# Optimization experiments

Hardware: AMD Instinct MI355X
Metric: run time of the kernel (lower is better)

Reference implementation:

```python
import jax, jax.numpy as jnp
import numpy as np


def setup_inputs() -> dict:
    key = jax.random.key(0)
    k1, k2 = jax.random.split(key)
    B, DIM, T, SIZE = 64, 512, 2048, 1024
    H = jax.random.normal(k1, (B, DIM, T), dtype=jnp.float32)
    units = jax.random.normal(k2, (DIM, SIZE), dtype=jnp.float32)
    return {"H": H, "units": units}


def reference(H, units):
    # H: (B, dim, T), units: (dim, size)
    # Original: C[b, s, t] = exp(-||H[b,:,t] - units[:,s]||^2) normalized over s.
    # exp(-d^2) / sum_s exp(-d^2) == softmax(-d^2, axis=s).
    Ht = jnp.swapaxes(H, 1, 2)                      # (B, T, dim)
    h_sq = jnp.sum(Ht * Ht, axis=-1, keepdims=True)  # (B, T, 1)
    m_sq = jnp.sum(units * units, axis=0)            # (size,)
    cross = jnp.einsum('btd,ds->bts', Ht, units)     # (B, T, size) GEMM
    sqdist = h_sq - 2.0 * cross + m_sq               # (B, T, size)
    C = jax.nn.softmax(-sqdist, axis=-1)             # normalize over codebook
    return jnp.swapaxes(C, 1, 2)                     # (B, size, T)
```

## Files before the change

### kernel.cpp

```cpp
#include <hip/hip_runtime.h>
#include <stdint.h>


typedef unsigned short u16;
typedef __attribute__((ext_vector_type(8))) short short8;
typedef __attribute__((ext_vector_type(4))) float f32x4;
typedef __attribute__((ext_vector_type(16))) float f32x16;

#define B_DIM 64
#define DIM   512
#define T_DIM 2048
#define S_DIM 1024

#define B_LO_O 65536
#define REDM_O 131072
#define REDS_O 133120
#define SM_SZ  135168

__device__ __forceinline__ u16 f32_to_bf16(float f) {
  uint32_t u = __float_as_uint(f);
  uint32_t r = u + 0x7FFFu + ((u >> 16) & 1u);
  return (u16)(r >> 16);
}
__device__ __forceinline__ float bf16_to_f32(u16 h) {
  return __uint_as_float(((uint32_t)h) << 16);
}

__global__ __launch_bounds__(256) void k_prep_units(const float* __restrict__ units,
                                                    u16* __restrict__ UpH, u16* __restrict__ UpL,
                                                    float* __restrict__ msq) {
  const int s0 = blockIdx.x * 4;
  const int tid = threadIdx.x;
  const int lane = tid & 63, wv = tid >> 6;
  float acc0 = 0.f, acc1 = 0.f, acc2 = 0.f, acc3 = 0.f;
#pragma unroll
  for (int j = 0; j < 2; ++j) {
    const int d = tid + j * 256;
    const float4 v = *(const float4*)(units + (size_t)d * S_DIM + s0);
    acc0 += v.x * v.x; acc1 += v.y * v.y; acc2 += v.z * v.z; acc3 += v.w * v.w;
    const int dbase = (d >> 4) * 16384 + ((d >> 3) & 1) * 256 + (d & 7);
    const float fv[4] = {v.x, v.y, v.z, v.w};
#pragma unroll
    for (int q = 0; q < 4; ++q) {
      const int s = s0 + q;
      const int idx = dbase + ((s >> 5) * 64 + (s & 31)) * 8;
      const u16 h = f32_to_bf16(fv[q]);
      UpH[idx] = h;
      UpL[idx] = f32_to_bf16(fv[q] - bf16_to_f32(h));
    }
  }
#pragma unroll
  for (int off = 1; off < 64; off <<= 1) {
    acc0 += __shfl_xor(acc0, off);
    acc1 += __shfl_xor(acc1, off);
    acc2 += __shfl_xor(acc2, off);
    acc3 += __shfl_xor(acc3, off);
  }
  __shared__ float part[4][4];
  if (lane == 0) { part[wv][0] = acc0; part[wv][1] = acc1; part[wv][2] = acc2; part[wv][3] = acc3; }
  __syncthreads();
  if (tid < 4) msq[s0 + tid] = part[0][tid] + part[1][tid] + part[2][tid] + part[3][tid];
}

__global__ __launch_bounds__(256) void k_prep_h(const float* __restrict__ H,
                                                u16* __restrict__ BpH, u16* __restrict__ BpL) {
  __shared__ float tile[64 * 68];
  const int bx = blockIdx.x;
  const int d0 = blockIdx.y * 64;
  const int b = blockIdx.z;
  const int t0 = bx * 64;
  const int tid = threadIdx.x;
#pragma unroll
  for (int j = 0; j < 4; ++j) {
    const int chunk = tid + j * 256;
    const int r = chunk >> 4, c4 = (chunk & 15) * 4;
    const float4 v = *(const float4*)(H + ((size_t)(b * DIM + d0 + r)) * T_DIM + t0 + c4);
    *(float4*)(&tile[r * 68 + c4]) = v;
  }
  __syncthreads();
#pragma unroll
  for (int j = 0; j < 2; ++j) {
    const int chunk = tid + j * 256;
    const int q = chunk >> 3, e8 = (chunk & 7) * 8;
    union { u16 us[8]; uint4 v4; } hi, lo;
#pragma unroll
    for (int k = 0; k < 8; ++k) {
      const float f = tile[(e8 + k) * 68 + q];
      const u16 h = f32_to_bf16(f);
      hi.us[k] = h;
      lo.us[k] = f32_to_bf16(f - bf16_to_f32(h));
    }
    const int dg = d0 + e8;
    const int chunkB = (q >> 5) * 64 + ((dg >> 3) & 1) * 32 + (q & 31);
    const size_t o = ((((size_t)b * 32 + bx) * 32 + (dg >> 4)) * 128 + chunkB) * 8;
    *(uint4*)(BpH + o) = hi.v4;
    *(uint4*)(BpL + o) = lo.v4;
  }
}

__device__ __forceinline__ void gl16(const void* g, void* l) {
  __builtin_amdgcn_global_load_lds((const __attribute__((address_space(1))) void*)g,
                                   (__attribute__((address_space(3))) void*)l, 16, 0, 0);
}

#define WAITV0() asm volatile("s_waitcnt vmcnt(0)" ::: "memory")
#define SYNCPT() do { __builtin_amdgcn_s_barrier(); __builtin_amdgcn_sched_barrier(0); } while (0)

__global__ __launch_bounds__(512, 2) void k_fused(const u16* __restrict__ UpH, const u16* __restrict__ UpL,
                                                  const u16* __restrict__ BpH, const u16* __restrict__ BpL,
                                                  const float* __restrict__ msq,
                                                  float* __restrict__ out) {
  __shared__ __align__(16) char sm[SM_SZ];
  const int tid = threadIdx.x;
  const int lane = tid & 63, wv = tid >> 6;
  const int l31 = lane & 31, lhi = lane >> 5;
  const int sw = wv;

  const int tgx = blockIdx.x;
  const int t00 = tgx * 64;
  const int bb = blockIdx.y;

  const char* const aH = (const char*)UpH + (sw * 4) * 1024 + lane * 16;
  const char* const aL = (const char*)UpL + (sw * 4) * 1024 + lane * 16;
  const size_t bgBase = (((size_t)bb * 32 + tgx) * 32) * 2048;
  const char* const pBH = (const char*)BpH + bgBase;
  const char* const pBL = (const char*)BpL + bgBase;

  f32x16 acc[4][2];
#pragma unroll
  for (int mt = 0; mt < 4; ++mt)
#pragma unroll
    for (int nt = 0; nt < 2; ++nt)
#pragma unroll
      for (int r = 0; r < 16; ++r)
        acc[mt][nt][r] = 0.f;

  short8 ah0[4], ah1[4], al0[4], al1[4];
  short8 bh0[2], bh1[2], bl0[2], bl1[2];

#define LD_AH(D, KS) do { const size_t ko = (size_t)(KS) * 32768;            \
    (D)[0] = *(const short8*)(aH + ko);                                      \
    (D)[1] = *(const short8*)(aH + ko + 1024);                               \
    (D)[2] = *(const short8*)(aH + ko + 2048);                               \
    (D)[3] = *(const short8*)(aH + ko + 3072); } while (0)
#define LD_AL(D, KS) do { const size_t ko = (size_t)(KS) * 32768;            \
    (D)[0] = *(const short8*)(aL + ko);                                      \
    (D)[1] = *(const short8*)(aL + ko + 1024);                               \
    (D)[2] = *(const short8*)(aL + ko + 2048);                               \
    (D)[3] = *(const short8*)(aL + ko + 3072); } while (0)
#define DS_B(BH, BL, KS) do { const int bo = (KS) * 2048 + lane * 16;        \
    (BH)[0] = *(const short8*)(sm + bo);                                     \
    (BH)[1] = *(const short8*)(sm + bo + 1024);                              \
    (BL)[0] = *(const short8*)(sm + B_LO_O + bo);                            \
    (BL)[1] = *(const short8*)(sm + B_LO_O + bo + 1024); } while (0)
#define STG(J) do { const int off = (16 + 2 * (J)) * 2048 + (wv & 3) * 1024 + lane * 16; \
    if (wv < 4) gl16(pBH + off, sm + off);                                   \
    else        gl16(pBL + off, sm + B_LO_O + off); } while (0)

#define MM8(AF, BF)                                                          \
    __builtin_amdgcn_s_setprio(1);                                           \
    _Pragma("unroll") for (int mt = 0; mt < 4; ++mt)                         \
      _Pragma("unroll") for (int nt = 0; nt < 2; ++nt)                       \
        acc[mt][nt] = __builtin_amdgcn_mfma_f32_32x32x16_bf16((AF)[mt], (BF)[nt], acc[mt][nt], 0, 0, 0); \
    __builtin_amdgcn_s_setprio(0);

#pragma unroll
  for (int r = 0; r < 4; ++r) {
    const int off = (tid + r * 512) * 16;
    gl16(pBH + off, sm + off);
    gl16(pBL + off, sm + B_LO_O + off);
  }
  LD_AH(ah0, 0); LD_AL(al0, 0);
  WAITV0();
  SYNCPT();
  DS_B(bh0, bl0, 0);
  LD_AH(ah1, 1); LD_AL(al1, 1);
  DS_B(bh1, bl1, 1);

#pragma unroll 1
  for (int k = 0; k < 32; k += 2) {
    if (k == 10) { WAITV0(); SYNCPT(); }
    const int kc2 = (k + 2 < 32) ? (k + 2) : 31;
    const int kc3 = (k + 3 < 32) ? (k + 3) : 31;
    if (k < 8) STG(k);
    MM8(ah0, bh0);
    MM8(ah0, bl0);
    MM8(al0, bh0);
    LD_AH(ah0, kc2); LD_AL(al0, kc2); DS_B(bh0, bl0, kc2);
    if (k + 1 < 8) STG(k + 1);
    MM8(ah1, bh1);
    MM8(ah1, bl1);
    MM8(al1, bh1);
    LD_AH(ah1, kc3); LD_AL(al1, kc3); DS_B(bh1, bl1, kc3);
  }

  float* redM = (float*)(sm + REDM_O);
  float* redS = (float*)(sm + REDS_O);
  float mx0 = -3.0e38f, mx1 = -3.0e38f;
#pragma unroll
  for (int mt = 0; mt < 4; ++mt) {
    const int sb = sw * 128 + mt * 32 + lhi * 4;
#pragma unroll
    for (int q = 0; q < 4; ++q) {
      const f32x4 mq = *(const f32x4*)(msq + sb + q * 8);
#pragma unroll
      for (int r = 0; r < 4; ++r) {
        const int reg = q * 4 + r;
        const float v0 = 2.f * acc[mt][0][reg] - mq[r];
        const float v1 = 2.f * acc[mt][1][reg] - mq[r];
        acc[mt][0][reg] = v0; acc[mt][1][reg] = v1;
        mx0 = fmaxf(mx0, v0); mx1 = fmaxf(mx1, v1);
      }
    }
  }
  mx0 = fmaxf(mx0, __shfl_xor(mx0, 32));
  mx1 = fmaxf(mx1, __shfl_xor(mx1, 32));
  if (lane < 32) { redM[wv * 64 + l31] = mx0; redM[wv * 64 + 32 + l31] = mx1; }
  __syncthreads();
  float M0 = redM[l31], M1 = redM[32 + l31];
#pragma unroll
  for (int w = 1; w < 8; ++w) {
    M0 = fmaxf(M0, redM[w * 64 + l31]);
    M1 = fmaxf(M1, redM[w * 64 + 32 + l31]);
  }
  float s0 = 0.f, s1 = 0.f;
#pragma unroll
  for (int mt = 0; mt < 4; ++mt)
#pragma unroll
    for (int reg = 0; reg < 16; ++reg) {
      const float e0 = __expf(acc[mt][0][reg] - M0);
      const float e1 = __expf(acc[mt][1][reg] - M1);
      acc[mt][0][reg] = e0; acc[mt][1][reg] = e1;
      s0 += e0; s1 += e1;
    }
  s0 += __shfl_xor(s0, 32);
  s1 += __shfl_xor(s1, 32);
  if (lane < 32) { redS[wv * 64 + l31] = s0; redS[wv * 64 + 32 + l31] = s1; }
  __syncthreads();
  float S0 = redS[l31], S1 = redS[32 + l31];
#pragma unroll
  for (int w = 1; w < 8; ++w) {
    S0 += redS[w * 64 + l31];
    S1 += redS[w * 64 + 32 + l31];
  }
  const float r0 = 1.0f / S0, r1 = 1.0f / S1;

  float* const outb = out + ((size_t)bb << 21);
  const int tc0 = t00 + l31, tc1 = t00 + 32 + l31;
#pragma unroll
  for (int mt = 0; mt < 4; ++mt) {
    const int sb = sw * 128 + mt * 32 + lhi * 4;
#pragma unroll
    for (int q = 0; q < 4; ++q)
#pragma unroll
      for (int r = 0; r < 4; ++r) {
        const int srow = sb + q * 8 + r;
        const int reg = q * 4 + r;
        outb[(size_t)srow * T_DIM + tc0] = acc[mt][0][reg] * r0;
        outb[(size_t)srow * T_DIM + tc1] = acc[mt][1][reg] * r1;
      }
  }
}

extern "C" void kernel_launch(void* const* d_in, const int* in_sizes, int n_in,
                              void* d_out, int out_size, void* d_ws, size_t ws_size,
                              hipStream_t stream) {
  (void)in_sizes; (void)n_in; (void)out_size; (void)ws_size;
  const float* H = (const float*)d_in[0];
  const float* units = (const float*)d_in[1];
  float* out = (float*)d_out;
  char* ws = (char*)d_ws;
  u16* BpH = (u16*)(ws);
  u16* BpL = (u16*)(ws + 134217728);
  u16* UpH = (u16*)(ws + 268435456);
  u16* UpL = (u16*)(ws + 269484032);
  float* msq = (float*)(ws + 270532608);

  k_prep_units<<<dim3(S_DIM / 4), 256, 0, stream>>>(units, UpH, UpL, msq);
  k_prep_h<<<dim3(T_DIM / 64, DIM / 64, B_DIM), 256, 0, stream>>>(H, BpH, BpL);
  k_fused<<<dim3(T_DIM / 64, B_DIM), 512, 0, stream>>>(UpH, UpL, BpH, BpL, msq, out);
}
```

Before: 577.8 us.

## Restructure K-loop into per-slab pipeline with fine-grained vmcnt waits

Replaces the double-buffered B fragments and the single full vmcnt(0) drain at k==10 with a per-slab schedule. Each slab syncs, reads its B fragment from LDS, issues the next LDS stage, waits on lgkm, and interleaves the next A global loads between the MFMA groups. Counted vmcnt waits let each slab wait only for its own data instead of draining every outstanding load. In exchange it adds a barrier per slab and drops the B register prefetch, so LDS read latency is exposed before each slab's MFMAs. Correctness depends on the hand-counted vmcnt values being right.

```diff
diff --git a/kernel.cpp b/kernel.cpp
--- a/kernel.cpp
+++ b/kernel.cpp
@@ -103,8 +103,9 @@
                                    (__attribute__((address_space(3))) void*)l, 16, 0, 0);
 }
 
-#define WAITV0() asm volatile("s_waitcnt vmcnt(0)" ::: "memory")
+#define WAITV(N) asm volatile("s_waitcnt vmcnt(" #N ")" ::: "memory")
 #define SYNCPT() do { __builtin_amdgcn_s_barrier(); __builtin_amdgcn_sched_barrier(0); } while (0)
+#define LGKM0()  do { asm volatile("s_waitcnt lgkmcnt(0)" ::: "memory"); __builtin_amdgcn_sched_barrier(0); } while (0)
 
 __global__ __launch_bounds__(512, 2) void k_fused(const u16* __restrict__ UpH, const u16* __restrict__ UpL,
                                                   const u16* __restrict__ BpH, const u16* __restrict__ BpL,
@@ -136,7 +137,7 @@
         acc[mt][nt][r] = 0.f;
 
   short8 ah0[4], ah1[4], al0[4], al1[4];
-  short8 bh0[2], bh1[2], bl0[2], bl1[2];
+  short8 bh[2], bl[2];
 
 #define LD_AH(D, KS) do { const size_t ko = (size_t)(KS) * 32768;            \
     (D)[0] = *(const short8*)(aH + ko);                                      \
@@ -148,12 +149,12 @@
     (D)[1] = *(const short8*)(aL + ko + 1024);                               \
     (D)[2] = *(const short8*)(aL + ko + 2048);                               \
     (D)[3] = *(const short8*)(aL + ko + 3072); } while (0)
-#define DS_B(BH, BL, KS) do { const int bo = (KS) * 2048 + lane * 16;        \
-    (BH)[0] = *(const short8*)(sm + bo);                                     \
-    (BH)[1] = *(const short8*)(sm + bo + 1024);                              \
-    (BL)[0] = *(const short8*)(sm + B_LO_O + bo);                            \
-    (BL)[1] = *(const short8*)(sm + B_LO_O + bo + 1024); } while (0)
-#define STG(J) do { const int off = (16 + 2 * (J)) * 2048 + (wv & 3) * 1024 + lane * 16; \
+#define DS_B(KS) do { const int bo = (KS) * 2048 + lane * 16;                \
+    bh[0] = *(const short8*)(sm + bo);                                       \
+    bh[1] = *(const short8*)(sm + bo + 1024);                                \
+    bl[0] = *(const short8*)(sm + B_LO_O + bo);                              \
+    bl[1] = *(const short8*)(sm + B_LO_O + bo + 1024); } while (0)
+#define STG(K) do { const int off = (16 + 2 * (K)) * 2048 + (wv & 3) * 1024 + lane * 16; \
     if (wv < 4) gl16(pBH + off, sm + off);                                   \
     else        gl16(pBL + off, sm + B_LO_O + off); } while (0)
 
@@ -164,6 +165,18 @@
         acc[mt][nt] = __builtin_amdgcn_mfma_f32_32x32x16_bf16((AF)[mt], (BF)[nt], acc[mt][nt], 0, 0, 0); \
     __builtin_amdgcn_s_setprio(0);
 
+#define SLAB(K, AH, AL, DO_STG, DO_LD) do {                                  \
+    SYNCPT();                                                                \
+    DS_B(K);                                                                 \
+    if (DO_STG) STG(K);                                                      \
+    LGKM0();                                                                 \
+    MM8(AH, bh);                                                             \
+    MM8(AH, bl);                                                             \
+    if (DO_LD) LD_AH(AH, (K) + 2);                                           \
+    MM8(AL, bh);                                                             \
+    if (DO_LD) LD_AL(AL, (K) + 2);                                           \
+  } while (0)
+
 #pragma unroll
   for (int r = 0; r < 4; ++r) {
     const int off = (tid + r * 512) * 16;
@@ -171,28 +184,25 @@
     gl16(pBL + off, sm + B_LO_O + off);
   }
   LD_AH(ah0, 0); LD_AL(al0, 0);
-  WAITV0();
-  SYNCPT();
-  DS_B(bh0, bl0, 0);
   LD_AH(ah1, 1); LD_AL(al1, 1);
-  DS_B(bh1, bl1, 1);
-
+  WAITV(16);
+
+  WAITV(8);  SLAB(0, ah0, al0, true, true);
+  WAITV(9);  SLAB(1, ah1, al1, true, true);
 #pragma unroll 1
-  for (int k = 0; k < 32; k += 2) {
-    if (k == 10) { WAITV0(); SYNCPT(); }
-    const int kc2 = (k + 2 < 32) ? (k + 2) : 31;
-    const int kc3 = (k + 3 < 32) ? (k + 3) : 31;
-    if (k < 8) STG(k);
-    MM8(ah0, bh0);
-    MM8(ah0, bl0);
-    MM8(al0, bh0);
-    LD_AH(ah0, kc2); LD_AL(al0, kc2); DS_B(bh0, bl0, kc2);
-    if (k + 1 < 8) STG(k + 1);
-    MM8(ah1, bh1);
-    MM8(ah1, bl1);
-    MM8(al1, bh1);
-    LD_AH(ah1, kc3); LD_AL(al1, kc3); DS_B(bh1, bl1, kc3);
-  }
+  for (int k = 2; k < 8; k += 2) {
+    WAITV(9);  SLAB(k,     ah0, al0, true, true);
+    WAITV(9);  SLAB(k + 1, ah1, al1, true, true);
+  }
+  WAITV(9);  SLAB(8, ah0, al0, false, true);
+#pragma unroll 1
+  for (int k = 9; k < 29; k += 2) {
+    WAITV(8);  SLAB(k,     ah1, al1, false, true);
+    WAITV(8);  SLAB(k + 1, ah0, al0, false, true);
+  }
+  WAITV(8);  SLAB(29, ah1, al1, false, true);
+  WAITV(8);  SLAB(30, ah0, al0, false, false);
+  WAITV(0);  SLAB(31, ah1, al1, false, false);
 
   float* redM = (float*)(sm + REDM_O);
   float* redS = (float*)(sm + REDS_O);
```

Result: faster. 560.4 us (-3.0%).

## Restructure GEMM main loop into phased pipeline with fine-grained vmcnt waits

Applied to the files above, without the earlier changes.

Rewrites the K loop as 16 phases. Each phase synchronises, reads both B k-slices from LDS up front, and issues the global loads for the next A fragments between MFMA groups, gated by explicit partial vmcnt waits instead of a single full drain. The aim is to overlap global A-fragment latency and LDS staging with MFMA work, and to avoid the full vmcnt(0) stall at the staging boundary. In exchange there is a workgroup barrier every phase, and correctness now depends on hand-counted outstanding-load numbers.

```diff
diff --git a/kernel.cpp b/kernel.cpp
--- a/kernel.cpp
+++ b/kernel.cpp
@@ -103,8 +103,9 @@
                                    (__attribute__((address_space(3))) void*)l, 16, 0, 0);
 }
 
-#define WAITV0() asm volatile("s_waitcnt vmcnt(0)" ::: "memory")
+#define WAITV(N) asm volatile("s_waitcnt vmcnt(" #N ")" ::: "memory")
 #define SYNCPT() do { __builtin_amdgcn_s_barrier(); __builtin_amdgcn_sched_barrier(0); } while (0)
+#define LGKM0()  do { asm volatile("s_waitcnt lgkmcnt(0)" ::: "memory"); __builtin_amdgcn_sched_barrier(0); } while (0)
 
 __global__ __launch_bounds__(512, 2) void k_fused(const u16* __restrict__ UpH, const u16* __restrict__ UpL,
                                                   const u16* __restrict__ BpH, const u16* __restrict__ BpL,
@@ -135,8 +136,8 @@
       for (int r = 0; r < 16; ++r)
         acc[mt][nt][r] = 0.f;
 
-  short8 ah0[4], ah1[4], al0[4], al1[4];
-  short8 bh0[2], bh1[2], bl0[2], bl1[2];
+  short8 ahA[4], alA[4], ahB[4], alB[4];
+  short8 bhA[2], blA[2], bhB[2], blB[2];
 
 #define LD_AH(D, KS) do { const size_t ko = (size_t)(KS) * 32768;            \
     (D)[0] = *(const short8*)(aH + ko);                                      \
@@ -148,7 +149,7 @@
     (D)[1] = *(const short8*)(aL + ko + 1024);                               \
     (D)[2] = *(const short8*)(aL + ko + 2048);                               \
     (D)[3] = *(const short8*)(aL + ko + 3072); } while (0)
-#define DS_B(BH, BL, KS) do { const int bo = (KS) * 2048 + lane * 16;        \
+#define DS_B2(BH, BL, KS) do { const int bo = (KS) * 2048 + lane * 16;       \
     (BH)[0] = *(const short8*)(sm + bo);                                     \
     (BH)[1] = *(const short8*)(sm + bo + 1024);                              \
     (BL)[0] = *(const short8*)(sm + B_LO_O + bo);                            \
@@ -164,35 +165,46 @@
         acc[mt][nt] = __builtin_amdgcn_mfma_f32_32x32x16_bf16((AF)[mt], (BF)[nt], acc[mt][nt], 0, 0, 0); \
     __builtin_amdgcn_s_setprio(0);
 
+#define PHASE(J, DO_STG, WN) do {                                            \
+    const int s0_ = 2 * (J), s1_ = 2 * (J) + 1;                              \
+    const int p0_ = (s0_ + 2 < 32) ? s0_ + 2 : 31;                           \
+    const int p1_ = (s1_ + 2 < 32) ? s1_ + 2 : 31;                           \
+    SYNCPT();                                                                \
+    DS_B2(bhA, blA, s0_);                                                    \
+    DS_B2(bhB, blB, s1_);                                                    \
+    if (DO_STG) STG(J);                                                      \
+    LGKM0();                                                                 \
+    WAITV(WN);                                                               \
+    MM8(ahA, bhA);                                                           \
+    MM8(ahA, blA);                                                           \
+    LD_AH(ahA, p0_);                                                         \
+    WAITV(WN);                                                               \
+    MM8(alA, bhA);                                                           \
+    LD_AL(alA, p0_);                                                         \
+    WAITV(WN);                                                               \
+    MM8(ahB, bhB);                                                           \
+    MM8(ahB, blB);                                                           \
+    LD_AH(ahB, p1_);                                                         \
+    WAITV(WN);                                                               \
+    MM8(alB, bhB);                                                           \
+    LD_AL(alB, p1_);                                                         \
+  } while (0)
+
 #pragma unroll
   for (int r = 0; r < 4; ++r) {
     const int off = (tid + r * 512) * 16;
     gl16(pBH + off, sm + off);
     gl16(pBL + off, sm + B_LO_O + off);
   }
-  LD_AH(ah0, 0); LD_AL(al0, 0);
-  WAITV0();
-  SYNCPT();
-  DS_B(bh0, bl0, 0);
-  LD_AH(ah1, 1); LD_AL(al1, 1);
-  DS_B(bh1, bl1, 1);
-
+  LD_AH(ahA, 0); LD_AL(alA, 0);
+  LD_AH(ahB, 1); LD_AL(alB, 1);
+  WAITV(16);
+
+  PHASE(0, true, 13);
 #pragma unroll 1
-  for (int k = 0; k < 32; k += 2) {
-    if (k == 10) { WAITV0(); SYNCPT(); }
-    const int kc2 = (k + 2 < 32) ? (k + 2) : 31;
-    const int kc3 = (k + 3 < 32) ? (k + 3) : 31;
-    if (k < 8) STG(k);
-    MM8(ah0, bh0);
-    MM8(ah0, bl0);
-    MM8(al0, bh0);
-    LD_AH(ah0, kc2); LD_AL(al0, kc2); DS_B(bh0, bl0, kc2);
-    if (k + 1 < 8) STG(k + 1);
-    MM8(ah1, bh1);
-    MM8(ah1, bl1);
-    MM8(al1, bh1);
-    LD_AH(ah1, kc3); LD_AL(al1, kc3); DS_B(bh1, bl1, kc3);
-  }
+  for (int j = 1; j < 8; ++j) PHASE(j, true, 13);
+#pragma unroll 1
+  for (int j = 8; j < 16; ++j) PHASE(j, false, 12);
 
   float* redM = (float*)(sm + REDM_O);
   float* redS = (float*)(sm + REDS_O);
```

Measured after the change: 559.1 us. 1.03x faster.

## Split fused GEMM-softmax block across 16 waves with simpler unpipelined K loop

Applied to the files above, without the earlier changes.

The fused kernel now launches 1024 threads (16 waves) per block, and each wave owns 64 codebook rows instead of 128, which halves the per-wave accumulator and fragment register footprint. The staged, double-buffered K loop with interleaved partial B loads is replaced by one upfront load of the whole B tile into LDS, followed by a plain loop that reads A from global and B from LDS every step. The aim is to hide latency through more resident waves instead of software pipelining. In exchange, loads and MFMAs inside each wave are no longer overlapped, and the softmax reductions now span 16 waves.

```diff
diff --git a/kernel.cpp b/kernel.cpp
--- a/kernel.cpp
+++ b/kernel.cpp
@@ -14,8 +14,8 @@
 
 #define B_LO_O 65536
 #define REDM_O 131072
-#define REDS_O 133120
-#define SM_SZ  135168
+#define REDS_O 135168
+#define SM_SZ  139264
 
 __device__ __forceinline__ u16 f32_to_bf16(float f) {
   uint32_t u = __float_as_uint(f);
@@ -106,10 +106,10 @@
 #define WAITV0() asm volatile("s_waitcnt vmcnt(0)" ::: "memory")
 #define SYNCPT() do { __builtin_amdgcn_s_barrier(); __builtin_amdgcn_sched_barrier(0); } while (0)
 
-__global__ __launch_bounds__(512, 2) void k_fused(const u16* __restrict__ UpH, const u16* __restrict__ UpL,
-                                                  const u16* __restrict__ BpH, const u16* __restrict__ BpL,
-                                                  const float* __restrict__ msq,
-                                                  float* __restrict__ out) {
+__global__ __launch_bounds__(1024, 4) void k_fused(const u16* __restrict__ UpH, const u16* __restrict__ UpL,
+                                                   const u16* __restrict__ BpH, const u16* __restrict__ BpL,
+                                                   const float* __restrict__ msq,
+                                                   float* __restrict__ out) {
   __shared__ __align__(16) char sm[SM_SZ];
   const int tid = threadIdx.x;
   const int lane = tid & 63, wv = tid >> 6;
@@ -120,86 +120,69 @@
   const int t00 = tgx * 64;
   const int bb = blockIdx.y;
 
-  const char* const aH = (const char*)UpH + (sw * 4) * 1024 + lane * 16;
-  const char* const aL = (const char*)UpL + (sw * 4) * 1024 + lane * 16;
-  const size_t bgBase = (((size_t)bb * 32 + tgx) * 32) * 2048;
+  const char* const aH = (const char*)UpH + sw * 2048 + lane * 16;
+  const char* const aL = (const char*)UpL + sw * 2048 + lane * 16;
+  const size_t bgBase = (size_t)(bb * 32 + tgx) * 65536;
   const char* const pBH = (const char*)BpH + bgBase;
   const char* const pBL = (const char*)BpL + bgBase;
 
-  f32x16 acc[4][2];
-#pragma unroll
-  for (int mt = 0; mt < 4; ++mt)
+#pragma unroll
+  for (int r = 0; r < 4; ++r) {
+    const int off = (tid + r * 1024) * 16;
+    gl16(pBH + off, sm + off);
+  }
+#pragma unroll
+  for (int r = 0; r < 4; ++r) {
+    const int off = (tid + r * 1024) * 16;
+    gl16(pBL + off, sm + B_LO_O + off);
+  }
+
+  f32x16 acc[2][2];
+#pragma unroll
+  for (int mt = 0; mt < 2; ++mt)
 #pragma unroll
     for (int nt = 0; nt < 2; ++nt)
 #pragma unroll
       for (int r = 0; r < 16; ++r)
         acc[mt][nt][r] = 0.f;
 
-  short8 ah0[4], ah1[4], al0[4], al1[4];
-  short8 bh0[2], bh1[2], bl0[2], bl1[2];
-
-#define LD_AH(D, KS) do { const size_t ko = (size_t)(KS) * 32768;            \
-    (D)[0] = *(const short8*)(aH + ko);                                      \
-    (D)[1] = *(const short8*)(aH + ko + 1024);                               \
-    (D)[2] = *(const short8*)(aH + ko + 2048);                               \
-    (D)[3] = *(const short8*)(aH + ko + 3072); } while (0)
-#define LD_AL(D, KS) do { const size_t ko = (size_t)(KS) * 32768;            \
-    (D)[0] = *(const short8*)(aL + ko);                                      \
-    (D)[1] = *(const short8*)(aL + ko + 1024);                               \
-    (D)[2] = *(const short8*)(aL + ko + 2048);                               \
-    (D)[3] = *(const short8*)(aL + ko + 3072); } while (0)
-#define DS_B(BH, BL, KS) do { const int bo = (KS) * 2048 + lane * 16;        \
-    (BH)[0] = *(const short8*)(sm + bo);                                     \
-    (BH)[1] = *(const short8*)(sm + bo + 1024);                              \
-    (BL)[0] = *(const short8*)(sm + B_LO_O + bo);                            \
-    (BL)[1] = *(const short8*)(sm + B_LO_O + bo + 1024); } while (0)
-#define STG(J) do { const int off = (16 + 2 * (J)) * 2048 + (wv & 3) * 1024 + lane * 16; \
-    if (wv < 4) gl16(pBH + off, sm + off);                                   \
-    else        gl16(pBL + off, sm + B_LO_O + off); } while (0)
-
-#define MM8(AF, BF)                                                          \
-    __builtin_amdgcn_s_setprio(1);                                           \
-    _Pragma("unroll") for (int mt = 0; mt < 4; ++mt)                         \
-      _Pragma("unroll") for (int nt = 0; nt < 2; ++nt)                       \
-        acc[mt][nt] = __builtin_amdgcn_mfma_f32_32x32x16_bf16((AF)[mt], (BF)[nt], acc[mt][nt], 0, 0, 0); \
-    __builtin_amdgcn_s_setprio(0);
-
-#pragma unroll
-  for (int r = 0; r < 4; ++r) {
-    const int off = (tid + r * 512) * 16;
-    gl16(pBH + off, sm + off);
-    gl16(pBL + off, sm + B_LO_O + off);
-  }
-  LD_AH(ah0, 0); LD_AL(al0, 0);
   WAITV0();
   SYNCPT();
-  DS_B(bh0, bl0, 0);
-  LD_AH(ah1, 1); LD_AL(al1, 1);
-  DS_B(bh1, bl1, 1);
 
 #pragma unroll 1
-  for (int k = 0; k < 32; k += 2) {
-    if (k == 10) { WAITV0(); SYNCPT(); }
-    const int kc2 = (k + 2 < 32) ? (k + 2) : 31;
-    const int kc3 = (k + 3 < 32) ? (k + 3) : 31;
-    if (k < 8) STG(k);
-    MM8(ah0, bh0);
-    MM8(ah0, bl0);
-    MM8(al0, bh0);
-    LD_AH(ah0, kc2); LD_AL(al0, kc2); DS_B(bh0, bl0, kc2);
-    if (k + 1 < 8) STG(k + 1);
-    MM8(ah1, bh1);
-    MM8(ah1, bl1);
-    MM8(al1, bh1);
-    LD_AH(ah1, kc3); LD_AL(al1, kc3); DS_B(bh1, bl1, kc3);
+  for (int ks = 0; ks < 32; ++ks) {
+    const int bo = ks * 2048 + lane * 16;
+    short8 bh0 = *(const short8*)(sm + bo);
+    short8 bh1 = *(const short8*)(sm + bo + 1024);
+    short8 bl0 = *(const short8*)(sm + B_LO_O + bo);
+    short8 bl1 = *(const short8*)(sm + B_LO_O + bo + 1024);
+    const size_t ko = (size_t)ks << 15;
+    short8 ah0 = *(const short8*)(aH + ko);
+    short8 ah1 = *(const short8*)(aH + ko + 1024);
+    short8 al0 = *(const short8*)(aL + ko);
+    short8 al1 = *(const short8*)(aL + ko + 1024);
+    __builtin_amdgcn_s_setprio(1);
+    acc[0][0] = __builtin_amdgcn_mfma_f32_32x32x16_bf16(ah0, bh0, acc[0][0], 0, 0, 0);
+    acc[0][1] = __builtin_amdgcn_mfma_f32_32x32x16_bf16(ah0, bh1, acc[0][1], 0, 0, 0);
+    acc[1][0] = __builtin_amdgcn_mfma_f32_32x32x16_bf16(ah1, bh0, acc[1][0], 0, 0, 0);
+    acc[1][1] = __builtin_amdgcn_mfma_f32_32x32x16_bf16(ah1, bh1, acc[1][1], 0, 0, 0);
+    acc[0][0] = __builtin_amdgcn_mfma_f32_32x32x16_bf16(ah0, bl0, acc[0][0], 0, 0, 0);
+    acc[0][1] = __builtin_amdgcn_mfma_f32_32x32x16_bf16(ah0, bl1, acc[0][1], 0, 0, 0);
+    acc[1][0] = __builtin_amdgcn_mfma_f32_32x32x16_bf16(ah1, bl0, acc[1][0], 0, 0, 0);
+    acc[1][1] = __builtin_amdgcn_mfma_f32_32x32x16_bf16(ah1, bl1, acc[1][1], 0, 0, 0);
+    acc[0][0] = __builtin_amdgcn_mfma_f32_32x32x16_bf16(al0, bh0, acc[0][0], 0, 0, 0);
+    acc[0][1] = __builtin_amdgcn_mfma_f32_32x32x16_bf16(al0, bh1, acc[0][1], 0, 0, 0);
+    acc[1][0] = __builtin_amdgcn_mfma_f32_32x32x16_bf16(al1, bh0, acc[1][0], 0, 0, 0);
+    acc[1][1] = __builtin_amdgcn_mfma_f32_32x32x16_bf16(al1, bh1, acc[1][1], 0, 0, 0);
+    __builtin_amdgcn_s_setprio(0);
   }
 
   float* redM = (float*)(sm + REDM_O);
   float* redS = (float*)(sm + REDS_O);
   float mx0 = -3.0e38f, mx1 = -3.0e38f;
 #pragma unroll
-  for (int mt = 0; mt < 4; ++mt) {
-    const int sb = sw * 128 + mt * 32 + lhi * 4;
+  for (int mt = 0; mt < 2; ++mt) {
+    const int sb = sw * 64 + mt * 32 + lhi * 4;
 #pragma unroll
     for (int q = 0; q < 4; ++q) {
       const f32x4 mq = *(const f32x4*)(msq + sb + q * 8);
@@ -219,13 +202,13 @@
   __syncthreads();
   float M0 = redM[l31], M1 = redM[32 + l31];
 #pragma unroll
-  for (int w = 1; w < 8; ++w) {
+  for (int w = 1; w < 16; ++w) {
     M0 = fmaxf(M0, redM[w * 64 + l31]);
     M1 = fmaxf(M1, redM[w * 64 + 32 + l31]);
   }
   float s0 = 0.f, s1 = 0.f;
 #pragma unroll
-  for (int mt = 0; mt < 4; ++mt)
+  for (int mt = 0; mt < 2; ++mt)
 #pragma unroll
     for (int reg = 0; reg < 16; ++reg) {
       const float e0 = __expf(acc[mt][0][reg] - M0);
@@ -239,7 +222,7 @@
   __syncthreads();
   float S0 = redS[l31], S1 = redS[32 + l31];
 #pragma unroll
-  for (int w = 1; w < 8; ++w) {
+  for (int w = 1; w < 16; ++w) {
     S0 += redS[w * 64 + l31];
     S1 += redS[w * 64 + 32 + l31];
   }
@@ -248,8 +231,8 @@
   float* const outb = out + ((size_t)bb << 21);
   const int tc0 = t00 + l31, tc1 = t00 + 32 + l31;
 #pragma unroll
-  for (int mt = 0; mt < 4; ++mt) {
-    const int sb = sw * 128 + mt * 32 + lhi * 4;
+  for (int mt = 0; mt < 2; ++mt) {
+    const int sb = sw * 64 + mt * 32 + lhi * 4;
 #pragma unroll
     for (int q = 0; q < 4; ++q)
 #pragma unroll
@@ -278,5 +261,5 @@
 
   k_prep_units<<<dim3(S_DIM / 4), 256, 0, stream>>>(units, UpH, UpL, msq);
   k_prep_h<<<dim3(T_DIM / 64, DIM / 64, B_DIM), 256, 0, stream>>>(H, BpH, BpL);
-  k_fused<<<dim3(T_DIM / 64, B_DIM), 512, 0, stream>>>(UpH, UpL, BpH, BpL, msq, out);
-}
+  k_fused<<<dim3(T_DIM / 64, B_DIM), 1024, 0, stream>>>(UpH, UpL, BpH, BpL, msq, out);
+}
```

Measured after the change: 597.0 us. 1.03x slower.
